# Kernel optimization log

Measured on AMD Instinct MI355X. Metric: run time of the kernel, lower is better.

Reference implementation:

```python
import jax, jax.numpy as jnp
import numpy as np

B, T, HID = 1, 2048, 2048
H = 16            # num_heads == num_key_value_heads
D = HID // H      # head_dim == feature_dim == 128
EPS = 1e-5


def _layer_norm(x, eps=1e-5):
    mu = jnp.mean(x, axis=-1, keepdims=True)
    var = jnp.mean((x - mu) ** 2, axis=-1, keepdims=True)
    return (x - mu) * jax.lax.rsqrt(var + eps)


def _feature_map(x, gamma, beta):
    # ReBased feature map, flatten=False (parallel mode): affine then LayerNorm
    return _layer_norm(x * gamma + beta)


def setup_inputs() -> dict:
    key = jax.random.key(0)
    ks = jax.random.split(key, 8)
    s = HID ** -0.5
    return {
        "hidden_states": jax.random.normal(ks[0], (B, T, HID), jnp.float32),
        "Wq": jax.random.normal(ks[1], (HID, HID), jnp.float32) * s,
        "Wk": jax.random.normal(ks[2], (HID, HID), jnp.float32) * s,
        "Wv": jax.random.normal(ks[3], (HID, HID), jnp.float32) * s,
        "Wo": jax.random.normal(ks[4], (HID, HID), jnp.float32) * s,
        "gamma": 1.0 + 0.1 * jax.random.normal(ks[5], (D,), jnp.float32),
        "beta": 0.1 * jax.random.normal(ks[6], (D,), jnp.float32),
    }


def reference(hidden_states, Wq, Wk, Wv, Wo, gamma, beta):
    b, t, _ = hidden_states.shape
    # projections (nn.Linear: x @ W.T), split into heads: [b, t, h, d]
    q = (hidden_states @ Wq.T).reshape(b, t, H, D)
    k = (hidden_states @ Wk.T).reshape(b, t, H, D)
    v = (hidden_states @ Wv.T).reshape(b, t, H, D)
    # ReBased feature map (no quadratic flatten in parallel mode)
    q = _feature_map(q, gamma, beta)
    k = _feature_map(k, gamma, beta)
    # parallel_rebased: scale q, quadratic score, causal mask, normalize
    q = q * (D ** -0.5)
    attn = jnp.einsum('bqhd,bkhd->bhqk', q, k) ** 2  # (q.k)^2
    mask = jnp.tril(jnp.ones((t, t), dtype=bool))
    attn = jnp.where(mask, attn, 0.0)
    o = jnp.einsum('bhqk,bkhd->bqhd', attn, v)       # [b, t, h, d]
    z = jnp.sum(attn, axis=-1)                       # [b, h, t]
    o = o / (jnp.swapaxes(z, 1, 2)[..., None] + EPS)
    o = o.reshape(b, t, H * D)
    return o @ Wo.T
```

## Files before the change

### kernel.cpp

```cpp
#include <hip/hip_runtime.h>
#include <hip/hip_bf16.h>
#include <stdint.h>

typedef __bf16 bf16;
typedef __bf16 v8bf __attribute__((ext_vector_type(8)));
typedef float  v4f  __attribute__((ext_vector_type(4)));

#define TSEQ   2048
#define HIDDIM 2048
#define NHEAD  16
#define HDIM   128

__device__ __forceinline__ void async16(void* lds, const void* g)
{
    __builtin_amdgcn_global_load_lds(
        (__attribute__((address_space(1))) void*)(uintptr_t)g,
        (__attribute__((address_space(3))) void*)(unsigned int)(uintptr_t)lds,
        16, 0, 0);
}

__global__ __launch_bounds__(256) void conv5(const float* __restrict__ s0, bf16* __restrict__ d0,
                                             const float* __restrict__ s1, bf16* __restrict__ d1,
                                             const float* __restrict__ s2, bf16* __restrict__ d2,
                                             const float* __restrict__ s3, bf16* __restrict__ d3,
                                             const float* __restrict__ s4, bf16* __restrict__ d4)
{
    const float* src; bf16* dst;
    switch (blockIdx.y) {
        case 0: src = s0; dst = d0; break;
        case 1: src = s1; dst = d1; break;
        case 2: src = s2; dst = d2; break;
        case 3: src = s3; dst = d3; break;
        default: src = s4; dst = d4; break;
    }
    const size_t i = ((size_t)blockIdx.x * 256 + threadIdx.x) * 8;
    const float4 a = *(const float4*)(src + i);
    const float4 b = *(const float4*)(src + i + 4);
    v8bf o;
    o[0] = (bf16)a.x; o[1] = (bf16)a.y; o[2] = (bf16)a.z; o[3] = (bf16)a.w;
    o[4] = (bf16)b.x; o[5] = (bf16)b.y; o[6] = (bf16)b.z; o[7] = (bf16)b.w;
    *(v8bf*)(dst + i) = o;
}


#define PBAR() do { __builtin_amdgcn_sched_barrier(0); __builtin_amdgcn_s_barrier(); \
                    __builtin_amdgcn_sched_barrier(0); } while (0)

#define STA(buf, ka) do { _Pragma("unroll") \
    for (int s_ = 0; s_ < 4; ++s_) \
        async16(&sA[(buf)*16384 + s_*4096 + w*512], \
                Ag + (ka) + (size_t)(s_*64 + w*8 + (l>>3))*2048); } while (0)
#define STB(buf, ka) do { _Pragma("unroll") \
    for (int s_ = 0; s_ < 3; ++s_) \
        async16(&sB[(buf)*12288 + s_*4096 + w*512], \
                Bg + (ka) + (size_t)(s_*64 + w*8 + (l>>3))*2048); } while (0)

#define RDA(buf, mh) do { _Pragma("unroll") \
    for (int mi_ = 0; mi_ < 4; ++mi_) { \
        const bf16* p_ = &sA[(buf)*16384 + (wm*128 + (mh)*64 + mi_*16 + lr)*64]; \
        a[mi_][0] = *(const v8bf*)(p_ + c0); \
        a[mi_][1] = *(const v8bf*)(p_ + c1); } } while (0)
#define RDB(buf) do { _Pragma("unroll") \
    for (int nj_ = 0; nj_ < 3; ++nj_) { \
        const bf16* p_ = &sB[(buf)*12288 + (wn*48 + nj_*16 + lr)*64]; \
        b[nj_][0] = *(const v8bf*)(p_ + c0); \
        b[nj_][1] = *(const v8bf*)(p_ + c1); } } while (0)

#define MQ24(mh) do { _Pragma("unroll") \
    for (int mi_ = 0; mi_ < 4; ++mi_) { _Pragma("unroll") \
        for (int nj_ = 0; nj_ < 3; ++nj_) { \
            acc[(mh)*4+mi_][nj_] = __builtin_amdgcn_mfma_f32_16x16x32_bf16( \
                a[mi_][0], b[nj_][0], acc[(mh)*4+mi_][nj_], 0, 0, 0); \
            acc[(mh)*4+mi_][nj_] = __builtin_amdgcn_mfma_f32_16x16x32_bf16( \
                a[mi_][1], b[nj_][1], acc[(mh)*4+mi_][nj_], 0, 0, 0); \
        } } } while (0)

__global__ __launch_bounds__(512, 2) void gemm_qkv192(const bf16* __restrict__ A,
    const bf16* __restrict__ Wcat, bf16* __restrict__ qb, bf16* __restrict__ kb,
    bf16* __restrict__ vb)
{
    __shared__ __attribute__((aligned(16))) bf16 sA[2*16384];
    __shared__ __attribute__((aligned(16))) bf16 sB[2*12288];
    const int n0g = blockIdx.x * 192;
    const int m0  = blockIdx.y * 256;

    const int tid = threadIdx.x, l = tid & 63, w = tid >> 6;
    const int wm = w >> 2, wn = w & 3;
    const int quad = l >> 4, lr = l & 15;
    const int scol = ((l & 7) ^ ((l >> 3) & 7)) * 8;
    const int c0 = ((quad    ) ^ (lr & 7)) * 8;
    const int c1 = ((quad + 4) ^ (lr & 7)) * 8;

    const bf16* Ag = A    + (size_t)m0  * 2048 + scol;
    const bf16* Bg = Wcat + (size_t)n0g * 2048 + scol;

    v4f  acc[8][3] = {};
    v8bf a[4][2], b[3][2];

    STA(0, 0); STB(0, 0);
    STB(1, 64); STA(1, 64);
    asm volatile("s_waitcnt vmcnt(7)" ::: "memory");
    __builtin_amdgcn_s_barrier();
    __builtin_amdgcn_sched_barrier(0);

#pragma unroll 1
    for (int it = 0; it < 16; ++it) {
        const int k2 = (it*128 + 128) & 2047;
        const int k3 = (it*128 + 192) & 2047;

        RDB(0); RDA(0, 0);
        PBAR(); __builtin_amdgcn_s_setprio(1); MQ24(0); __builtin_amdgcn_s_setprio(0); PBAR();
        RDA(0, 1);
        STB(0, k2);
        PBAR(); __builtin_amdgcn_s_setprio(1); MQ24(1); __builtin_amdgcn_s_setprio(0);
        asm volatile("s_waitcnt vmcnt(3)" ::: "memory");
        PBAR();
        RDB(1); RDA(1, 0);
        STA(0, k2);
        PBAR(); __builtin_amdgcn_s_setprio(1); MQ24(0); __builtin_amdgcn_s_setprio(0); PBAR();
        RDA(1, 1);
        STB(1, k3); STA(1, k3);
        PBAR(); __builtin_amdgcn_s_setprio(1); MQ24(1); __builtin_amdgcn_s_setprio(0);
        asm volatile("s_waitcnt vmcnt(7)" ::: "memory");
        PBAR();
    }
    asm volatile("s_waitcnt vmcnt(0)" ::: "memory");

#pragma unroll
    for (int mi = 0; mi < 8; ++mi) {
        const int row = m0 + wm*128 + (mi >> 2)*64 + (mi & 3)*16 + quad*4;
#pragma unroll
        for (int nj = 0; nj < 3; ++nj) {
            const int colg  = n0g + wn*48 + nj*16;
            const int which = colg >> 11;
            bf16* Cb = (which == 0) ? qb : (which == 1) ? kb : vb;
            const int lcol = (colg & 2047) + lr;
#pragma unroll
            for (int r = 0; r < 4; ++r)
                Cb[(size_t)(row + r)*2048 + lcol] = (bf16)acc[mi][nj][r];
        }
    }
}

__global__ __launch_bounds__(256) void gemm_out(const bf16* __restrict__ A,
    const bf16* __restrict__ B, float* __restrict__ C)
{
    __shared__ __attribute__((aligned(16))) bf16 sA[128*32];
    __shared__ __attribute__((aligned(16))) bf16 sB[64*32];
    const int m0 = blockIdx.y * 128, n0 = blockIdx.x * 64;
    const int K = HIDDIM, ldc = HIDDIM;
    const int tid  = threadIdx.x;
    const int lane = tid & 63;
    const int w    = tid >> 6;
    const int wm   = w >> 1, wn = w & 1;
    const int quad = lane >> 4, lr = lane & 15;
    const int srow = lane >> 2;
    const int scol = (lane & 3) * 8;

    const bf16* gA0 = A + (size_t)(m0 + w*32 + srow) * K + scol;
    const bf16* gB0 = B + (size_t)(n0 + w*16 + srow) * K + scol;
    bf16* lA0 = &sA[w*1024];
    bf16* lB0 = &sB[w*512];

    v4f acc[4][2] = {};

    for (int kt = 0; kt < K; kt += 32) {
        __syncthreads();
        async16(lA0,       gA0 + kt);
        async16(lA0 + 512, gA0 + (size_t)16*K + kt);
        async16(lB0,       gB0 + kt);
        __syncthreads();
        v8bf a[4], b[2];
#pragma unroll
        for (int i = 0; i < 4; ++i)
            a[i] = *(const v8bf*)&sA[(wm*64 + i*16 + lr)*32 + quad*8];
#pragma unroll
        for (int j = 0; j < 2; ++j)
            b[j] = *(const v8bf*)&sB[(wn*32 + j*16 + lr)*32 + quad*8];
#pragma unroll
        for (int i = 0; i < 4; ++i)
#pragma unroll
            for (int j = 0; j < 2; ++j)
                acc[i][j] = __builtin_amdgcn_mfma_f32_16x16x32_bf16(a[i], b[j], acc[i][j], 0, 0, 0);
    }

#pragma unroll
    for (int i = 0; i < 4; ++i) {
        const int row_b = m0 + wm*64 + i*16 + quad*4;
#pragma unroll
        for (int j = 0; j < 2; ++j) {
            const int col = n0 + wn*32 + j*16 + lr;
#pragma unroll
            for (int r = 0; r < 4; ++r)
                C[(size_t)(row_b + r)*ldc + col] = acc[i][j][r];
        }
    }
}

__global__ __launch_bounds__(256) void fmap(bf16* __restrict__ qb, bf16* __restrict__ kb,
                                            const float* __restrict__ gamma,
                                            const float* __restrict__ beta)
{
    const int rid  = blockIdx.x * 4 + (threadIdx.x >> 6);
    const int lane = threadIdx.x & 63;
    bf16* base = (rid < TSEQ*NHEAD) ? (qb + (size_t)rid * HDIM)
                                    : (kb + (size_t)(rid - TSEQ*NHEAD) * HDIM);
    const float scale = (rid < TSEQ*NHEAD) ? 0.08838834764831845f : 1.0f;

    const bf16 x0b = base[lane*2], x1b = base[lane*2+1];
    const float g0 = gamma[lane*2], g1 = gamma[lane*2+1];
    const float b0 = beta[lane*2],  b1 = beta[lane*2+1];
    float x0 = (float)x0b*g0 + b0;
    float x1 = (float)x1b*g1 + b1;
    float s  = x0 + x1;
    float sq = x0*x0 + x1*x1;
#pragma unroll
    for (int off = 1; off < 64; off <<= 1) { s += __shfl_xor(s, off); sq += __shfl_xor(sq, off); }
    const float mu   = s * (1.0f/128.0f);
    float var        = sq * (1.0f/128.0f) - mu*mu;
    var = fmaxf(var, 0.0f);
    const float rstd = rsqrtf(var + 1e-5f);
    base[lane*2]   = (bf16)((x0 - mu) * rstd * scale);
    base[lane*2+1] = (bf16)((x1 - mu) * rstd * scale);
}

__global__ __launch_bounds__(256) void transpose2048(const bf16* __restrict__ src,
                                                     bf16* __restrict__ dst)
{
    __shared__ __attribute__((aligned(16))) bf16 tile[64][72];
    const int t0 = blockIdx.y * 64, c0 = blockIdx.x * 64;
    const int tid = threadIdx.x;
    const int r = tid >> 3;
    const int c = (tid & 7) * 8;
#pragma unroll
    for (int p = 0; p < 2; ++p) {
        const int rr = r + p*32;
        *(v8bf*)&tile[rr][c] = *(const v8bf*)(src + (size_t)(t0+rr)*HIDDIM + c0 + c);
    }
    __syncthreads();
#pragma unroll
    for (int p = 0; p < 2; ++p) {
        const int orow = r + p*32;
        v8bf o;
#pragma unroll
        for (int i = 0; i < 8; ++i) o[i] = tile[c + i][orow];
        *(v8bf*)(dst + (size_t)(c0+orow)*HIDDIM + t0 + c) = o;
    }
}

__global__ __launch_bounds__(512, 2) void attn(const bf16* __restrict__ qb,
                                               const bf16* __restrict__ kb,
                                               const bf16* __restrict__ vt,
                                               bf16* __restrict__ ob)
{
    __shared__ __attribute__((aligned(16))) bf16 sK[2*64*136];
    __shared__ __attribute__((aligned(16))) bf16 sV[2*128*72];
    __shared__ __attribute__((aligned(16))) bf16 sS[2*64*72];
    __shared__ __attribute__((aligned(16))) float sO[64*129];
    __shared__ __attribute__((aligned(16))) float sZ[64*17];

    const int h    = blockIdx.y;
    const int pr   = blockIdx.x;
    const int tid  = threadIdx.x, lane = tid & 63;
    const int w    = tid >> 6;
    const int g    = w >> 2;
    const int ww   = w & 3;
    const int quad = lane >> 4, lr = lane & 15;
    const int rs   = tid >> 4;
    const int cs   = (tid & 15) * 8;

#pragma unroll
    for (int ti = 0; ti < 2; ++ti) {
        const int tile = ti ? pr : (31 - pr);
        const int nch  = tile + 1;

        v8bf qa[4];
        {
            const bf16* q0 = qb + (size_t)(tile*64 + ww*16 + lr)*HIDDIM + h*HDIM + quad*8;
#pragma unroll
            for (int ks = 0; ks < 4; ++ks)
                qa[ks] = *(const v8bf*)(q0 + ks*32);
        }

        v4f  o[8] = {};
        float z[4] = {0.f, 0.f, 0.f, 0.f};

        v8bf curK[4], curV[4], nxtK[4], nxtV[4];
#pragma unroll
        for (int p = 0; p < 4; ++p) {
            curK[p] = *(const v8bf*)(kb + (size_t)(rs + p*32)*HIDDIM + h*HDIM + cs);
            curV[p] = *(const v8bf*)(vt + (size_t)(h*HDIM + rs + p*32)*HIDDIM + cs);
        }

        for (int ich = 0; ich < nch; ich += 2) {
            __syncthreads();
#pragma unroll
            for (int p = 0; p < 4; ++p) {
                const int r = rs + p*32;
                *(v8bf*)&sK[(r>>6)*8704 + (r&63)*136 + cs] = curK[p];
            }
#pragma unroll
            for (int p = 0; p < 4; ++p)
                *(v8bf*)&sV[(cs>>6)*9216 + (rs + p*32)*72 + (cs & 63)] = curV[p];

            if (ich + 2 < nch) {
                const int s1 = (ich + 2) * 64;
#pragma unroll
                for (int p = 0; p < 4; ++p) {
                    nxtK[p] = *(const v8bf*)(kb + (size_t)(s1 + rs + p*32)*HIDDIM + h*HDIM + cs);
                    nxtV[p] = *(const v8bf*)(vt + (size_t)(h*HDIM + rs + p*32)*HIDDIM + s1 + cs);
                }
            }
            __syncthreads();

            const int ch = ich + g;
            if (ch < nch) {
                const bf16* sKg = &sK[g*8704];
                const bf16* sVg = &sV[g*9216];
                bf16*       sSg = &sS[g*4608];
                const bool  diag = (ch == tile);
                const int   s0   = ch * 64;

                v8bf kbf[4][4];
#pragma unroll
                for (int nj = 0; nj < 4; ++nj)
#pragma unroll
                    for (int ks = 0; ks < 4; ++ks)
                        kbf[nj][ks] = *(const v8bf*)&sKg[(nj*16 + lr)*136 + ks*32 + quad*8];
                const int row_l = ww*16 + quad*4;
                const int qg    = tile*64 + row_l;
#pragma unroll
                for (int nj = 0; nj < 4; ++nj) {
                    v4f s4 = {0.f, 0.f, 0.f, 0.f};
#pragma unroll
                    for (int ks = 0; ks < 4; ++ks)
                        s4 = __builtin_amdgcn_mfma_f32_16x16x32_bf16(qa[ks], kbf[nj][ks], s4, 0, 0, 0);
                    const int col = nj*16 + lr;
                    const int sg  = s0 + col;
#pragma unroll
                    for (int r = 0; r < 4; ++r) {
                        float val = s4[r] * s4[r];
                        if (diag && (sg > qg + r)) val = 0.0f;
                        const bf16 vb16 = (bf16)val;
                        z[r] += (float)vb16;
                        sSg[(row_l + r)*72 + col] = vb16;
                    }
                }

#pragma unroll
                for (int ks = 0; ks < 2; ++ks) {
                    const v8bf sa = *(const v8bf*)&sSg[(ww*16 + lr)*72 + ks*32 + quad*8];
#pragma unroll
                    for (int nd = 0; nd < 8; ++nd) {
                        const v8bf vbf = *(const v8bf*)&sVg[(nd*16 + lr)*72 + ks*32 + quad*8];
                        o[nd] = __builtin_amdgcn_mfma_f32_16x16x32_bf16(sa, vbf, o[nd], 0, 0, 0);
                    }
                }
            }

            if (ich + 2 < nch) {
#pragma unroll
                for (int p = 0; p < 4; ++p) { curK[p] = nxtK[p]; curV[p] = nxtV[p]; }
            }
        }

        const int row_l = ww*16 + quad*4;
        __syncthreads();
        if (g == 1) {
#pragma unroll
            for (int nd = 0; nd < 8; ++nd)
#pragma unroll
                for (int r = 0; r < 4; ++r)
                    sO[(row_l + r)*129 + nd*16 + lr] = o[nd][r];
#pragma unroll
            for (int r = 0; r < 4; ++r)
                sZ[(row_l + r)*17 + lr] = z[r];
        }
        __syncthreads();
        if (g == 0) {
#pragma unroll
            for (int nd = 0; nd < 8; ++nd)
#pragma unroll
                for (int r = 0; r < 4; ++r)
                    o[nd][r] += sO[(row_l + r)*129 + nd*16 + lr];
#pragma unroll
            for (int r = 0; r < 4; ++r) {
                float zz = z[r] + sZ[(row_l + r)*17 + lr];
                zz += __shfl_xor(zz, 1); zz += __shfl_xor(zz, 2);
                zz += __shfl_xor(zz, 4); zz += __shfl_xor(zz, 8);
                z[r] = zz + 1e-5f;
            }
            const size_t rbase = (size_t)(tile*64 + row_l)*HIDDIM + h*HDIM;
#pragma unroll
            for (int nd = 0; nd < 8; ++nd) {
                const int col = nd*16 + lr;
#pragma unroll
                for (int r = 0; r < 4; ++r)
                    ob[rbase + (size_t)r*HIDDIM + col] = (bf16)(o[nd][r] / z[r]);
            }
        }
    }
}

extern "C" void kernel_launch(void* const* d_in, const int* in_sizes, int n_in,
                              void* d_out, int out_size, void* d_ws, size_t ws_size,
                              hipStream_t stream)
{
    const float* hs    = (const float*)d_in[0];
    const float* Wq    = (const float*)d_in[1];
    const float* Wk    = (const float*)d_in[2];
    const float* Wv    = (const float*)d_in[3];
    const float* Wo    = (const float*)d_in[4];
    const float* gamma = (const float*)d_in[5];
    const float* beta  = (const float*)d_in[6];
    float* outp = (float*)d_out;

    const size_t MAT = (size_t)TSEQ * HIDDIM;

    bf16* ws   = (bf16*)d_ws;
    bf16* hs_b = ws + 0*MAT;
    bf16* vt   = hs_b;
    bf16* Wq_b = ws + 1*MAT;
    bf16* Wk_b = ws + 2*MAT;
    bf16* Wv_b = ws + 3*MAT;
    bf16* Wo_b = ws + 4*MAT;
    bf16* vb   = ws + 5*MAT;
    bf16* ob   = vb;
    bf16* qb   = (bf16*)d_out;
    bf16* kb   = (bf16*)d_out + MAT;

    conv5<<<dim3(2048, 5), 256, 0, stream>>>(hs, hs_b, Wq, Wq_b, Wk, Wk_b, Wv, Wv_b, Wo, Wo_b);
    gemm_qkv192<<<dim3(32, 8), 512, 0, stream>>>(hs_b, Wq_b, qb, kb, vb);
    fmap<<<dim3(2*TSEQ*NHEAD/4), 256, 0, stream>>>(qb, kb, gamma, beta);
    transpose2048<<<dim3(32, 32), 256, 0, stream>>>(vb, vt);
    attn<<<dim3(16, 16), 512, 0, stream>>>(qb, kb, vt, ob);
    gemm_out<<<dim3(32, 16), 256, 0, stream>>>(ob, Wo_b, outp);
}
```

Baseline: 272.9 us.

## Reshape QKV GEMM tile to 128x384 with finer-grained load pipeline

New measurement: 269.4 us. About the same (-1.3%).

```diff
diff --git a/kernel.cpp b/kernel.cpp
--- a/kernel.cpp
+++ b/kernel.cpp
@@ -46,43 +46,42 @@
 #define PBAR() do { __builtin_amdgcn_sched_barrier(0); __builtin_amdgcn_s_barrier(); \
                     __builtin_amdgcn_sched_barrier(0); } while (0)
 
-#define STA(buf, ka) do { _Pragma("unroll") \
-    for (int s_ = 0; s_ < 4; ++s_) \
-        async16(&sA[(buf)*16384 + s_*4096 + w*512], \
-                Ag + (ka) + (size_t)(s_*64 + w*8 + (l>>3))*2048); } while (0)
-#define STB(buf, ka) do { _Pragma("unroll") \
-    for (int s_ = 0; s_ < 3; ++s_) \
-        async16(&sB[(buf)*12288 + s_*4096 + w*512], \
-                Bg + (ka) + (size_t)(s_*64 + w*8 + (l>>3))*2048); } while (0)
-
-#define RDA(buf, mh) do { _Pragma("unroll") \
+#define STU(ldst, gsrc) do { \
+    async16((ldst) + w*512,        (gsrc) + (size_t)(w*8 + (l>>3))*2048); \
+    async16((ldst) + 4096 + w*512, (gsrc) + (size_t)(64 + w*8 + (l>>3))*2048); \
+} while (0)
+
+#define RDA(buf) do { _Pragma("unroll") \
     for (int mi_ = 0; mi_ < 4; ++mi_) { \
-        const bf16* p_ = &sA[(buf)*16384 + (wm*128 + (mh)*64 + mi_*16 + lr)*64]; \
+        const bf16* p_ = &sA[(buf)*8192 + (wm*64 + mi_*16 + lr)*64]; \
         a[mi_][0] = *(const v8bf*)(p_ + c0); \
         a[mi_][1] = *(const v8bf*)(p_ + c1); } } while (0)
-#define RDB(buf) do { _Pragma("unroll") \
-    for (int nj_ = 0; nj_ < 3; ++nj_) { \
-        const bf16* p_ = &sB[(buf)*12288 + (wn*48 + nj_*16 + lr)*64]; \
+
+#define RDB(buf, nh) do { _Pragma("unroll") \
+    for (int nj_ = 0; nj_ < 2; ++nj_) { \
+        const bf16* p_ = &sB[(buf)*24576 + ((nh)*128 + wn*32 + nj_*16 + lr)*64]; \
         b[nj_][0] = *(const v8bf*)(p_ + c0); \
         b[nj_][1] = *(const v8bf*)(p_ + c1); } } while (0)
 
-#define MQ24(mh) do { _Pragma("unroll") \
+#define MQ(nh) do { _Pragma("unroll") \
     for (int mi_ = 0; mi_ < 4; ++mi_) { _Pragma("unroll") \
-        for (int nj_ = 0; nj_ < 3; ++nj_) { \
-            acc[(mh)*4+mi_][nj_] = __builtin_amdgcn_mfma_f32_16x16x32_bf16( \
-                a[mi_][0], b[nj_][0], acc[(mh)*4+mi_][nj_], 0, 0, 0); \
-            acc[(mh)*4+mi_][nj_] = __builtin_amdgcn_mfma_f32_16x16x32_bf16( \
-                a[mi_][1], b[nj_][1], acc[(mh)*4+mi_][nj_], 0, 0, 0); \
+        for (int nj_ = 0; nj_ < 2; ++nj_) { \
+            acc[mi_][(nh)*2+nj_] = __builtin_amdgcn_mfma_f32_16x16x32_bf16( \
+                a[mi_][0], b[nj_][0], acc[mi_][(nh)*2+nj_], 0, 0, 0); \
+            acc[mi_][(nh)*2+nj_] = __builtin_amdgcn_mfma_f32_16x16x32_bf16( \
+                a[mi_][1], b[nj_][1], acc[mi_][(nh)*2+nj_], 0, 0, 0); \
         } } } while (0)
 
-__global__ __launch_bounds__(512, 2) void gemm_qkv192(const bf16* __restrict__ A,
+#define VMC(n) asm volatile("s_waitcnt vmcnt(" #n ")" ::: "memory")
+
+__global__ __launch_bounds__(512, 2) void gemm_qkv384(const bf16* __restrict__ A,
     const bf16* __restrict__ Wcat, bf16* __restrict__ qb, bf16* __restrict__ kb,
     bf16* __restrict__ vb)
 {
-    __shared__ __attribute__((aligned(16))) bf16 sA[2*16384];
-    __shared__ __attribute__((aligned(16))) bf16 sB[2*12288];
-    const int n0g = blockIdx.x * 192;
-    const int m0  = blockIdx.y * 256;
+    __shared__ __attribute__((aligned(16))) bf16 sA[2*8192];
+    __shared__ __attribute__((aligned(16))) bf16 sB[2*24576];
+    const int n0g = blockIdx.x * 384;
+    const int m0  = blockIdx.y * 128;
 
     const int tid = threadIdx.x, l = tid & 63, w = tid >> 6;
     const int wm = w >> 2, wn = w & 3;
@@ -94,50 +93,67 @@
     const bf16* Ag = A    + (size_t)m0  * 2048 + scol;
     const bf16* Bg = Wcat + (size_t)n0g * 2048 + scol;
 
-    v4f  acc[8][3] = {};
-    v8bf a[4][2], b[3][2];
-
-    STA(0, 0); STB(0, 0);
-    STB(1, 64); STA(1, 64);
-    asm volatile("s_waitcnt vmcnt(7)" ::: "memory");
+    v4f  acc[4][6] = {};
+    v8bf a[4][2], b[2][2];
+
+    STU(&sA[0],           Ag);
+    STU(&sB[0],           Bg);
+    STU(&sB[8192],        Bg + (size_t)128*2048);
+    STU(&sB[16384],       Bg + (size_t)256*2048);
+    STU(&sA[8192],        Ag + 64);
+    STU(&sB[24576],       Bg + 64);
+    STU(&sB[24576+8192],  Bg + (size_t)128*2048 + 64);
+    VMC(10);
     __builtin_amdgcn_s_barrier();
     __builtin_amdgcn_sched_barrier(0);
 
 #pragma unroll 1
     for (int it = 0; it < 16; ++it) {
+        const int k1 =  it*128 + 64;
         const int k2 = (it*128 + 128) & 2047;
         const int k3 = (it*128 + 192) & 2047;
 
-        RDB(0); RDA(0, 0);
-        PBAR(); __builtin_amdgcn_s_setprio(1); MQ24(0); __builtin_amdgcn_s_setprio(0); PBAR();
-        RDA(0, 1);
-        STB(0, k2);
-        PBAR(); __builtin_amdgcn_s_setprio(1); MQ24(1); __builtin_amdgcn_s_setprio(0);
-        asm volatile("s_waitcnt vmcnt(3)" ::: "memory");
-        PBAR();
-        RDB(1); RDA(1, 0);
-        STA(0, k2);
-        PBAR(); __builtin_amdgcn_s_setprio(1); MQ24(0); __builtin_amdgcn_s_setprio(0); PBAR();
-        RDA(1, 1);
-        STB(1, k3); STA(1, k3);
-        PBAR(); __builtin_amdgcn_s_setprio(1); MQ24(1); __builtin_amdgcn_s_setprio(0);
-        asm volatile("s_waitcnt vmcnt(7)" ::: "memory");
-        PBAR();
+        RDA(0); RDB(0, 0);
+        STU(&sB[24576+16384], Bg + (size_t)256*2048 + k1);
+        PBAR(); __builtin_amdgcn_s_setprio(1); MQ(0); __builtin_amdgcn_s_setprio(0);
+        VMC(10); PBAR();
+        RDB(0, 1);
+        STU(&sA[0], Ag + k2);
+        STU(&sB[0], Bg + k2);
+        PBAR(); __builtin_amdgcn_s_setprio(1); MQ(1); __builtin_amdgcn_s_setprio(0);
+        VMC(12); PBAR();
+        RDB(0, 2);
+        STU(&sB[8192], Bg + (size_t)128*2048 + k2);
+        PBAR(); __builtin_amdgcn_s_setprio(1); MQ(2); __builtin_amdgcn_s_setprio(0);
+        VMC(10); PBAR();
+        RDA(1); RDB(1, 0);
+        STU(&sB[16384], Bg + (size_t)256*2048 + k2);
+        PBAR(); __builtin_amdgcn_s_setprio(1); MQ(0); __builtin_amdgcn_s_setprio(0);
+        VMC(10); PBAR();
+        RDB(1, 1);
+        STU(&sA[8192],  Ag + k3);
+        STU(&sB[24576], Bg + k3);
+        PBAR(); __builtin_amdgcn_s_setprio(1); MQ(1); __builtin_amdgcn_s_setprio(0);
+        VMC(12); PBAR();
+        RDB(1, 2);
+        STU(&sB[24576+8192], Bg + (size_t)128*2048 + k3);
+        PBAR(); __builtin_amdgcn_s_setprio(1); MQ(2); __builtin_amdgcn_s_setprio(0);
+        VMC(10); PBAR();
     }
     asm volatile("s_waitcnt vmcnt(0)" ::: "memory");
 
 #pragma unroll
-    for (int mi = 0; mi < 8; ++mi) {
-        const int row = m0 + wm*128 + (mi >> 2)*64 + (mi & 3)*16 + quad*4;
-#pragma unroll
-        for (int nj = 0; nj < 3; ++nj) {
-            const int colg  = n0g + wn*48 + nj*16;
+    for (int mi = 0; mi < 4; ++mi) {
+        const int row = m0 + wm*64 + mi*16 + quad*4;
+#pragma unroll
+        for (int j = 0; j < 6; ++j) {
+            const int colg  = n0g + (j >> 1)*128 + wn*32 + (j & 1)*16;
             const int which = colg >> 11;
             bf16* Cb = (which == 0) ? qb : (which == 1) ? kb : vb;
             const int lcol = (colg & 2047) + lr;
 #pragma unroll
             for (int r = 0; r < 4; ++r)
-                Cb[(size_t)(row + r)*2048 + lcol] = (bf16)acc[mi][nj][r];
+                Cb[(size_t)(row + r)*2048 + lcol] = (bf16)acc[mi][j][r];
         }
     }
 }
@@ -430,7 +446,7 @@
     bf16* kb   = (bf16*)d_out + MAT;
 
     conv5<<<dim3(2048, 5), 256, 0, stream>>>(hs, hs_b, Wq, Wq_b, Wk, Wk_b, Wv, Wv_b, Wo, Wo_b);
-    gemm_qkv192<<<dim3(32, 8), 512, 0, stream>>>(hs_b, Wq_b, qb, kb, vb);
+    gemm_qkv384<<<dim3(16, 16), 512, 0, stream>>>(hs_b, Wq_b, qb, kb, vb);
     fmap<<<dim3(2*TSEQ*NHEAD/4), 256, 0, stream>>>(qb, kb, gamma, beta);
     transpose2048<<<dim3(32, 32), 256, 0, stream>>>(vb, vt);
     attn<<<dim3(16, 16), 512, 0, stream>>>(qb, kb, vt, ob);
```
